# Kernel tuning notes

Hardware: AMD Instinct MI355X
Metric: run time of the kernel (lower is better)

The kernel has to match this reference:

```python
import jax, jax.numpy as jnp
import numpy as np

N, C_IN, H, W = 32, 3, 224, 224
C_OUT, K, STRIDE, PAD = 64, 3, 1, 1


def setup_inputs() -> dict:
    key = jax.random.key(0)
    k1, k2 = jax.random.split(key)
    x = jax.random.normal(k1, (N, C_IN, H, W), dtype=jnp.float32)
    weight = jax.random.normal(k2, (C_OUT, C_IN, K, K), dtype=jnp.float32)
    bias = jnp.zeros((C_OUT,), dtype=jnp.float32)
    return {"x": x, "weight": weight, "bias": bias}


def reference(x, weight, bias):
    # Equivalent to the manual im2col + GEMM: a standard 2D convolution
    # (cross-correlation, as the torch code slides the raw kernel).
    out = jax.lax.conv_general_dilated(
        x, weight,
        window_strides=(STRIDE, STRIDE),
        padding=[(PAD, PAD), (PAD, PAD)],
        dimension_numbers=("NCHW", "OIHW", "NCHW"),
    )
    return out + bias[None, :, None, None]
```

## Files before the change

kernel.cpp:

```cpp
#include <hip/hip_runtime.h>


#define N_IMG 32
#define C_IN 3
#define H_ 224
#define W_ 224
#define C_OUT 64
#define NPIX (H_ * W_)
#define COB 16

__global__ __launch_bounds__(256) void conv3x3_kernel(
    const float* __restrict__ x,
    const float* __restrict__ wgt,
    const float* __restrict__ bias,
    float* __restrict__ out)
{
    const int p = blockIdx.x * 256 + threadIdx.x;
    const int n = blockIdx.y;
    const int h = p / W_;
    const int w = p - h * W_;

    float in_v[27];
    const float* xn = x + (size_t)n * C_IN * NPIX;
#pragma unroll
    for (int ci = 0; ci < 3; ++ci) {
#pragma unroll
        for (int dh = 0; dh < 3; ++dh) {
            const int hh = h + dh - 1;
            const bool hok = (unsigned)hh < (unsigned)H_;
#pragma unroll
            for (int dw = 0; dw < 3; ++dw) {
                const int ww = w + dw - 1;
                const bool ok = hok && ((unsigned)ww < (unsigned)W_);
                in_v[(ci * 3 + dh) * 3 + dw] =
                    ok ? xn[ci * NPIX + hh * W_ + ww] : 0.0f;
            }
        }
    }

    float* outp = out + (size_t)n * C_OUT * NPIX + p;
#pragma unroll
    for (int cb = 0; cb < C_OUT / COB; ++cb) {
        float acc[COB];
#pragma unroll
        for (int i = 0; i < COB; ++i) acc[i] = bias[cb * COB + i];
#pragma unroll
        for (int i = 0; i < COB; ++i) {
            const float* wp = wgt + (size_t)(cb * COB + i) * 27;
#pragma unroll
            for (int k = 0; k < 27; ++k) acc[i] += in_v[k] * wp[k];
        }
#pragma unroll
        for (int i = 0; i < COB; ++i)
            outp[(size_t)(cb * COB + i) * NPIX] = acc[i];
    }
}

extern "C" void kernel_launch(void* const* d_in, const int* in_sizes, int n_in,
                              void* d_out, int out_size, void* d_ws, size_t ws_size,
                              hipStream_t stream) {
    const float* x    = (const float*)d_in[0];
    const float* wgt  = (const float*)d_in[1];
    const float* bias = (const float*)d_in[2];
    float* out = (float*)d_out;

    dim3 grid(NPIX / 256, N_IMG);
    dim3 block(256);
    conv3x3_kernel<<<grid, block, 0, stream>>>(x, wgt, bias, out);
}
```

Measured before the change: 456.8 us.

## Compute four adjacent pixels per thread with float4 loads and stores

Each thread now computes four horizontally adjacent output pixels. It loads a 6-wide input window per row using a float4 plus two halo scalars, and writes float4 outputs for each of the 64 output channels. Each weight load is now shared across four FMAs and memory accesses are wider, which should cut the instruction and load overhead per output. In exchange the grid has a quarter as many threads, and there are more registers per thread, which may lower occupancy.

```diff
diff --git a/kernel.cpp b/kernel.cpp
--- a/kernel.cpp
+++ b/kernel.cpp
@@ -7,52 +7,65 @@
 #define W_ 224
 #define C_OUT 64
 #define NPIX (H_ * W_)
-#define COB 16
+#define PIX_PER_THREAD 4
 
-__global__ __launch_bounds__(256) void conv3x3_kernel(
+__global__ __launch_bounds__(256) void conv3x3_p4(
     const float* __restrict__ x,
     const float* __restrict__ wgt,
     const float* __restrict__ bias,
     float* __restrict__ out)
 {
-    const int p = blockIdx.x * 256 + threadIdx.x;
-    const int n = blockIdx.y;
-    const int h = p / W_;
-    const int w = p - h * W_;
+    const int t  = blockIdx.x * 256 + threadIdx.x;
+    const int p0 = t * PIX_PER_THREAD;
+    const int n  = blockIdx.y;
+    const int h  = p0 / W_;
+    const int w0 = p0 - h * W_;
 
-    float in_v[27];
     const float* xn = x + (size_t)n * C_IN * NPIX;
+    const bool wl = (w0 > 0);
+    const bool wr = (w0 + 4 < W_);
+
+    float in_v[9][6];
 #pragma unroll
     for (int ci = 0; ci < 3; ++ci) {
 #pragma unroll
         for (int dh = 0; dh < 3; ++dh) {
+            const int r  = ci * 3 + dh;
             const int hh = h + dh - 1;
             const bool hok = (unsigned)hh < (unsigned)H_;
-#pragma unroll
-            for (int dw = 0; dw < 3; ++dw) {
-                const int ww = w + dw - 1;
-                const bool ok = hok && ((unsigned)ww < (unsigned)W_);
-                in_v[(ci * 3 + dh) * 3 + dw] =
-                    ok ? xn[ci * NPIX + hh * W_ + ww] : 0.0f;
+            const float* rowp = xn + ci * NPIX + hh * W_;
+            in_v[r][0] = (hok && wl) ? rowp[w0 - 1] : 0.0f;
+            if (hok) {
+                const float4 m = *(const float4*)(rowp + w0);
+                in_v[r][1] = m.x; in_v[r][2] = m.y;
+                in_v[r][3] = m.z; in_v[r][4] = m.w;
+            } else {
+                in_v[r][1] = 0.0f; in_v[r][2] = 0.0f;
+                in_v[r][3] = 0.0f; in_v[r][4] = 0.0f;
             }
+            in_v[r][5] = (hok && wr) ? rowp[w0 + 4] : 0.0f;
         }
     }
 
-    float* outp = out + (size_t)n * C_OUT * NPIX + p;
+    float* outp = out + (size_t)n * C_OUT * NPIX + p0;
+#pragma unroll 2
+    for (int c = 0; c < C_OUT; ++c) {
+        const float* wp = wgt + c * 27;
+        const float b = bias[c];
+        float a0 = b, a1 = b, a2 = b, a3 = b;
 #pragma unroll
-    for (int cb = 0; cb < C_OUT / COB; ++cb) {
-        float acc[COB];
+        for (int r = 0; r < 9; ++r) {
 #pragma unroll
-        for (int i = 0; i < COB; ++i) acc[i] = bias[cb * COB + i];
-#pragma unroll
-        for (int i = 0; i < COB; ++i) {
-            const float* wp = wgt + (size_t)(cb * COB + i) * 27;
-#pragma unroll
-            for (int k = 0; k < 27; ++k) acc[i] += in_v[k] * wp[k];
+            for (int dw = 0; dw < 3; ++dw) {
+                const float wv = wp[r * 3 + dw];
+                a0 = fmaf(in_v[r][dw + 0], wv, a0);
+                a1 = fmaf(in_v[r][dw + 1], wv, a1);
+                a2 = fmaf(in_v[r][dw + 2], wv, a2);
+                a3 = fmaf(in_v[r][dw + 3], wv, a3);
+            }
         }
-#pragma unroll
-        for (int i = 0; i < COB; ++i)
-            outp[(size_t)(cb * COB + i) * NPIX] = acc[i];
+        const float4 o = make_float4(a0, a1, a2, a3);
+        *(float4*)(outp + (size_t)c * NPIX) = o;
     }
 }
 
@@ -64,7 +77,7 @@
     const float* bias = (const float*)d_in[2];
     float* out = (float*)d_out;
 
-    dim3 grid(NPIX / 256, N_IMG);
+    dim3 grid(NPIX / (256 * PIX_PER_THREAD), N_IMG);
     dim3 block(256);
-    conv3x3_kernel<<<grid, block, 0, stream>>>(x, wgt, bias, out);
+    conv3x3_p4<<<grid, block, 0, stream>>>(x, wgt, bias, out);
 }
```

Result: slower. 494.2 us (+8.2%).
